# Kernel tuning notes

Hardware: AMD Instinct MI355X
Metric: run time of the kernel (lower is better)

The kernel has to match this reference:

```python
import jax, jax.numpy as jnp
import numpy as np

B, L, C, H, W = 4, 4096, 1024, 16, 512
D = C // H            # head_dim = 64
STRIDE = W // 2


def setup_inputs() -> dict:
    key = jax.random.key(0)
    k0, k1, k2 = jax.random.split(key, 3)
    s = 0.02
    return {
        "x": jax.random.normal(k0, (B, L, C), jnp.float32),
        "w_qkv": jax.random.normal(k1, (C, 3 * C), jnp.float32) * s,
        "b_qkv": jnp.zeros((3 * C,), jnp.float32),
        "w_out": jax.random.normal(k2, (C, C), jnp.float32) * s,
        "b_out": jnp.zeros((C,), jnp.float32),
    }


def _local_attention(x, w_qkv, b_qkv, w_out, b_out):
    b, l, c = x.shape
    pad = (-l) % W  # pad seq to multiple of window_size (0 here)
    x = jnp.pad(x, ((0, 0), (0, pad), (0, 0)))
    lp = l + pad
    qkv = (x @ w_qkv + b_qkv).reshape(b, lp, 3, H, D).transpose(2, 0, 3, 1, 4)
    q, k, v = qkv[0], qkv[1], qkv[2]  # each [B, H, Lp, D]
    nw = (lp - W) // STRIDE + 1       # number of overlapping windows
    # window token indices [nw, W]
    idx = jnp.arange(nw)[:, None] * STRIDE + jnp.arange(W)[None, :]
    qw = q[:, :, idx, :]  # [B, H, nw, W, D]
    kw = k[:, :, idx, :]
    vw = v[:, :, idx, :]
    # non-causal (bidirectional=True) attention within each window,
    # flash-attn default softmax scale = head_dim**-0.5
    scores = jnp.einsum('bhnqd,bhnkd->bhnqk', qw, kw) / jnp.sqrt(jnp.float32(D))
    probs = jax.nn.softmax(scores, axis=-1)
    ow = jnp.einsum('bhnqk,bhnkd->bhnqd', probs, vw)  # [B, H, nw, W, D]
    # concatenate window outputs along sequence, back to [B, nw*W, C]
    o = ow.transpose(0, 2, 3, 1, 4).reshape(b, nw * W, c)
    o = o @ w_out + b_out
    return o[:, :l, :]


def reference(x, w_qkv, b_qkv, w_out, b_out):
    return _local_attention(x, w_qkv, b_qkv, w_out, b_out)
```

## Files before the change

### kernel.cpp

```cpp
#include <hip/hip_runtime.h>

#define LQ 2304

typedef __attribute__((ext_vector_type(8))) short bf16x8;
typedef __attribute__((ext_vector_type(8))) unsigned short u16x8;
typedef __attribute__((ext_vector_type(4))) float f32x4;
typedef __attribute__((ext_vector_type(4))) unsigned int u32x4;

#define MFMA(a, b, c) __builtin_amdgcn_mfma_f32_16x16x32_bf16((a), (b), (c), 0, 0, 0)
#define AS1 __attribute__((address_space(1)))
#define AS3 __attribute__((address_space(3)))

static __device__ __forceinline__ unsigned short f2bf(float f) {
  unsigned int u = __builtin_bit_cast(unsigned int, f);
  u += 0x7fffu + ((u >> 16) & 1u);
  return (unsigned short)(u >> 16);
}

static __device__ __forceinline__ unsigned int pkbf(float hi, float lo) {
  return __builtin_amdgcn_perm(__builtin_bit_cast(unsigned int, hi),
                               __builtin_bit_cast(unsigned int, lo), 0x07060302u);
}

static __device__ __forceinline__ void lds16(const unsigned short* g, unsigned short* l) {
  __builtin_amdgcn_global_load_lds((AS1 const unsigned int*)g, (AS3 unsigned int*)l, 16, 0, 0);
}

static __device__ __forceinline__ void transpose_body(const float* __restrict__ src,
                                                      unsigned short* __restrict__ dst,
                                                      int K, int N, int bx, int by, int tid,
                                                      float (*t)[33]) {
  int bn = bx * 32, bk = by * 32;
  int tx = tid & 31, ty = tid >> 5;
  for (int i = ty; i < 32; i += 8)
    t[i][tx] = src[(size_t)(bk + i) * N + bn + tx];
  __syncthreads();
  for (int i = ty; i < 32; i += 8)
    dst[(size_t)(bn + i) * K + bk + tx] = f2bf(t[tx][i]);
}

__global__ __launch_bounds__(256) void preprocess(const float* __restrict__ x,
                                                  unsigned short* __restrict__ xbf,
                                                  const float* __restrict__ wqkv,
                                                  unsigned short* __restrict__ wqkvT,
                                                  const float* __restrict__ wout,
                                                  unsigned short* __restrict__ woutT) {
  __shared__ float t[32][33];
  int bid = blockIdx.x, tid = threadIdx.x;
  if (bid < 4608) {
    int idx = bid * 256 + tid;
    int b = idx / 294912;
    int g = idx - b * 294912;
    int row = g >> 7, c8 = (g & 127) * 8;
    const float* src = x + ((size_t)b * 4096 + row) * 1024 + c8;
    float4 f0 = *(const float4*)src;
    float4 f1 = *(const float4*)(src + 4);
    u16x8 u;
    u[0] = f2bf(f0.x); u[1] = f2bf(f0.y); u[2] = f2bf(f0.z); u[3] = f2bf(f0.w);
    u[4] = f2bf(f1.x); u[5] = f2bf(f1.y); u[6] = f2bf(f1.z); u[7] = f2bf(f1.w);
    *(u16x8*)(xbf + ((size_t)b * 2304 + row) * 1024 + c8) = u;
  } else if (bid < 7680) {
    int tb = bid - 4608;
    transpose_body(wqkv, wqkvT, 1024, 3072, tb % 96, tb / 96, tid, t);
  } else {
    int tb = bid - 7680;
    transpose_body(wout, woutT, 1024, 1024, tb & 31, tb >> 5, tid, t);
  }
}

#define K2SCALE 0.18033688011112042f
__global__ __launch_bounds__(256) void qkv_gemm(const unsigned short* __restrict__ xbf,
                                                const float* __restrict__ bqkv,
                                                const unsigned short* __restrict__ wT,
                                                unsigned short* __restrict__ qws,
                                                unsigned short* __restrict__ kws,
                                                unsigned short* __restrict__ vws) {
  __shared__ __align__(16) unsigned short As[128 * 64];
  __shared__ __align__(16) unsigned short Bs[128 * 64];
  const int tid = threadIdx.x;
  const int mt = blockIdx.y;
  const int nt = blockIdx.x;
  const int bidx = mt / 18;
  const int l0 = (mt % 18) * 128;
  const int n0 = nt * 128;
  const int lane = tid & 63, wv = tid >> 6;
  const int wm = (wv >> 1) * 64, wn = (wv & 1) * 64;
  const int l16 = lane & 15, quad = lane >> 4;

  const int srow = lane >> 3;
  const int sc = ((lane & 7) ^ srow) * 8;
  const unsigned short* ga = xbf + ((size_t)(bidx * LQ + l0 + wv * 32 + srow)) * 1024 + sc;
  const unsigned short* gb = wT + ((size_t)(n0 + wv * 32 + srow)) * 1024 + sc;
  unsigned short* la = As + wv * 2048;
  unsigned short* lb = Bs + wv * 2048;
  const int xsw = (l16 & 7) * 8;

  const f32x4 zero4 = {0.f, 0.f, 0.f, 0.f};
  f32x4 acc[4][4];
#pragma unroll
  for (int i = 0; i < 4; i++)
#pragma unroll
    for (int j = 0; j < 4; j++) acc[i][j] = zero4;

  for (int k0 = 0; k0 < 1024; k0 += 64) {
    __syncthreads();
#pragma unroll
    for (int j = 0; j < 4; j++) {
      lds16(ga + j * 8 * 1024, la + j * 512);
      lds16(gb + j * 8 * 1024, lb + j * 512);
    }
    __syncthreads();
#pragma unroll
    for (int h = 0; h < 2; h++) {
      bf16x8 af[4], bfv[4];
#pragma unroll
      for (int i = 0; i < 4; i++)
        af[i] = *(const bf16x8*)(&As[(wm + i * 16 + l16) * 64 + (((h << 5) + quad * 8) ^ xsw)]);
#pragma unroll
      for (int j = 0; j < 4; j++)
        bfv[j] = *(const bf16x8*)(&Bs[(wn + j * 16 + l16) * 64 + (((h << 5) + quad * 8) ^ xsw)]);
#pragma unroll
      for (int i = 0; i < 4; i++)
#pragma unroll
        for (int j = 0; j < 4; j++)
          acc[i][j] = MFMA(af[i], bfv[j], acc[i][j]);
    }
    ga += 64;
    gb += 64;
  }

#pragma unroll
  for (int j = 0; j < 4; j++) {
    int col = n0 + wn + j * 16 + l16;
    int which = col >> 10;
    int hcol = (col >> 6) & 15;
    int dcol = col & 63;
    unsigned short* dst = which == 0 ? qws : (which == 1 ? kws : vws);
    float scale = which == 0 ? K2SCALE : 1.0f;
    float bias = bqkv[col];
    size_t cbase = ((size_t)bidx * 16 + hcol) * LQ * 64 + dcol;
#pragma unroll
    for (int i = 0; i < 4; i++) {
      int lrow = l0 + wm + i * 16 + quad * 4;
#pragma unroll
      for (int r = 0; r < 4; r++)
        dst[cbase + (size_t)(lrow + r) * 64] = f2bf((acc[i][j][r] + bias) * scale);
    }
  }
}

#define KSTR 72
#define VSTRT 136

__global__ __launch_bounds__(512, 2) void attn_kernel(const unsigned short* __restrict__ q,
                                                      const unsigned short* __restrict__ k,
                                                      const unsigned short* __restrict__ v,
                                                      unsigned short* __restrict__ o) {
  __shared__ __align__(16) unsigned short Ks[128 * KSTR];
  __shared__ __align__(16) unsigned short Vt[64 * VSTRT];
  const int n = blockIdx.x, h = blockIdx.y, b = blockIdx.z;
  const size_t base = (((size_t)b * 16 + h) * LQ + n * 256) * 64;
  const unsigned short* qg = q + base;
  const unsigned short* kg = k + base;
  const unsigned short* vg = v + base;
  const int tid = threadIdx.x;
  const int lane = tid & 63, wv = tid >> 6;
  const int l16 = lane & 15, quad = lane >> 4;
  const f32x4 zero4 = {0.f, 0.f, 0.f, 0.f};
  const float RB = 0.002815015607053277f;

  bf16x8 qf0[4], qf1[4];
#pragma unroll
  for (int qs = 0; qs < 4; qs++) {
    int qrow = wv * 64 + qs * 16 + l16;
    qf0[qs] = *(const bf16x8*)(qg + (size_t)qrow * 64 + quad * 8);
    qf1[qs] = *(const bf16x8*)(qg + (size_t)qrow * 64 + quad * 8 + 32);
  }
  f32x4 O[4][4];
#pragma unroll
  for (int qs = 0; qs < 4; qs++)
#pragma unroll
    for (int dt = 0; dt < 4; dt++) O[qs][dt] = zero4;
  float lsum[4] = {0.f, 0.f, 0.f, 0.f};

  for (int kt = 0; kt < 4; kt++) {
    __syncthreads();
#pragma unroll
    for (int it = 0; it < 2; it++) {
      int i = it * 512 + tid;
      int key = i >> 3, part = i & 7;
      *(u16x8*)(&Ks[key * KSTR + part * 8]) =
          *(const u16x8*)(kg + (size_t)(kt * 128 + key) * 64 + part * 8);
    }
#pragma unroll
    for (int it = 0; it < 2; it++) {
      int key = it * 64 + lane;
      u16x8 raw = *(const u16x8*)(vg + (size_t)(kt * 128 + key) * 64 + wv * 8);
      int pos = (key & ~31) + ((key >> 2) & 3) * 8 + ((key >> 4) & 1) * 4 + (key & 3);
#pragma unroll
      for (int t = 0; t < 8; t++) Vt[(wv * 8 + t) * VSTRT + pos] = raw[t];
    }
    __syncthreads();

    for (int c = 0; c < 4; c++) {
      const unsigned short* kr0 = &Ks[(c * 32 + l16) * KSTR + quad * 8];
      bf16x8 ka0 = *(const bf16x8*)kr0;
      bf16x8 ka1 = *(const bf16x8*)(kr0 + 32);
      bf16x8 kb0 = *(const bf16x8*)(kr0 + 16 * KSTR);
      bf16x8 kb1 = *(const bf16x8*)(kr0 + 16 * KSTR + 32);
      bf16x8 vf[4];
#pragma unroll
      for (int dt = 0; dt < 4; dt++)
        vf[dt] = *(const bf16x8*)(&Vt[(dt * 16 + l16) * VSTRT + c * 32 + quad * 8]);
#pragma unroll
      for (int qs = 0; qs < 4; qs++) {
        f32x4 s0 = zero4, s1 = zero4;
        s0 = MFMA(ka0, qf0[qs], s0);
        s0 = MFMA(ka1, qf1[qs], s0);
        s1 = MFMA(kb0, qf0[qs], s1);
        s1 = MFMA(kb1, qf1[qs], s1);
        float p0[4], p1[4], ls = 0.f;
#pragma unroll
        for (int r = 0; r < 4; r++) {
          p0[r] = __builtin_amdgcn_exp2f(s0[r] + RB);
          p1[r] = __builtin_amdgcn_exp2f(s1[r] + RB);
          ls += p0[r] + p1[r];
        }
        lsum[qs] += ls;
        u32x4 pw;
        pw[0] = pkbf(p0[1], p0[0]);
        pw[1] = pkbf(p0[3], p0[2]);
        pw[2] = pkbf(p1[1], p1[0]);
        pw[3] = pkbf(p1[3], p1[2]);
        bf16x8 pf = __builtin_bit_cast(bf16x8, pw);
#pragma unroll
        for (int dt = 0; dt < 4; dt++)
          O[qs][dt] = MFMA(pf, vf[dt], O[qs][dt]);
      }
    }
  }

#pragma unroll
  for (int qs = 0; qs < 4; qs++) {
    float ls = lsum[qs];
    ls += __shfl_xor(ls, 16);
    ls += __shfl_xor(ls, 32);
    float linv = 1.0f / ls;
    float li[4];
#pragma unroll
    for (int r = 0; r < 4; r++) li[r] = __shfl(linv, quad * 4 + r);
    size_t orow = (size_t)b * 4096 + n * 512 + wv * 64 + qs * 16;
#pragma unroll
    for (int dt = 0; dt < 4; dt++) {
      int col = h * 64 + dt * 16 + l16;
#pragma unroll
      for (int r = 0; r < 4; r++)
        o[(orow + quad * 4 + r) * 1024 + col] = f2bf(O[qs][dt][r] * li[r]);
    }
  }
}

__global__ __launch_bounds__(256) void out_gemm(const unsigned short* __restrict__ A,
                                                const unsigned short* __restrict__ wT,
                                                const float* __restrict__ bout,
                                                float* __restrict__ out) {
  __shared__ __align__(16) unsigned short As[128 * 64];
  __shared__ __align__(16) unsigned short Bs[128 * 64];
  const int tid = threadIdx.x;
  const int m0 = blockIdx.y * 128;
  const int n0 = blockIdx.x * 128;
  const int lane = tid & 63, wv = tid >> 6;
  const int wm = (wv >> 1) * 64, wn = (wv & 1) * 64;
  const int l16 = lane & 15, quad = lane >> 4;

  const int srow = lane >> 3;
  const int sc = ((lane & 7) ^ srow) * 8;
  const unsigned short* ga = A + ((size_t)(m0 + wv * 32 + srow)) * 1024 + sc;
  const unsigned short* gb = wT + ((size_t)(n0 + wv * 32 + srow)) * 1024 + sc;
  unsigned short* la = As + wv * 2048;
  unsigned short* lb = Bs + wv * 2048;
  const int xsw = (l16 & 7) * 8;

  const f32x4 zero4 = {0.f, 0.f, 0.f, 0.f};
  f32x4 acc[4][4];
#pragma unroll
  for (int i = 0; i < 4; i++)
#pragma unroll
    for (int j = 0; j < 4; j++) acc[i][j] = zero4;

  for (int k0 = 0; k0 < 1024; k0 += 64) {
    __syncthreads();
#pragma unroll
    for (int j = 0; j < 4; j++) {
      lds16(ga + j * 8 * 1024, la + j * 512);
      lds16(gb + j * 8 * 1024, lb + j * 512);
    }
    __syncthreads();
#pragma unroll
    for (int h = 0; h < 2; h++) {
      bf16x8 af[4], bfv[4];
#pragma unroll
      for (int i = 0; i < 4; i++)
        af[i] = *(const bf16x8*)(&As[(wm + i * 16 + l16) * 64 + (((h << 5) + quad * 8) ^ xsw)]);
#pragma unroll
      for (int j = 0; j < 4; j++)
        bfv[j] = *(const bf16x8*)(&Bs[(wn + j * 16 + l16) * 64 + (((h << 5) + quad * 8) ^ xsw)]);
#pragma unroll
      for (int i = 0; i < 4; i++)
#pragma unroll
        for (int j = 0; j < 4; j++)
          acc[i][j] = MFMA(af[i], bfv[j], acc[i][j]);
    }
    ga += 64;
    gb += 64;
  }

#pragma unroll
  for (int j = 0; j < 4; j++) {
    int col = n0 + wn + j * 16 + l16;
    float bias = bout[col];
#pragma unroll
    for (int i = 0; i < 4; i++) {
      int row = m0 + wm + i * 16 + quad * 4;
#pragma unroll
      for (int r = 0; r < 4; r++)
        out[(size_t)(row + r) * 1024 + col] = acc[i][j][r] + bias;
    }
  }
}

#define WQKVT_OFF 0u
#define WOUTT_OFF (WQKVT_OFF + 3072u * 1024u * 2u)
#define QWS_OFF   (WOUTT_OFF + 1024u * 1024u * 2u)
#define KVQ_SZ    (4u * 16u * 2304u * 64u * 2u)
#define KWS_OFF   (QWS_OFF + KVQ_SZ)
#define VWS_OFF   (KWS_OFF + KVQ_SZ)
#define OWS_OFF   (VWS_OFF + KVQ_SZ)
#define XBF_OFF   OWS_OFF

extern "C" void kernel_launch(void* const* d_in, const int* in_sizes, int n_in,
                              void* d_out, int out_size, void* d_ws, size_t ws_size,
                              hipStream_t stream) {
  const float* x     = (const float*)d_in[0];
  const float* w_qkv = (const float*)d_in[1];
  const float* b_qkv = (const float*)d_in[2];
  const float* w_out = (const float*)d_in[3];
  const float* b_out = (const float*)d_in[4];
  float* out = (float*)d_out;
  char* ws = (char*)d_ws;

  unsigned short* wqkvT = (unsigned short*)(ws + WQKVT_OFF);
  unsigned short* woutT = (unsigned short*)(ws + WOUTT_OFF);
  unsigned short* qws   = (unsigned short*)(ws + QWS_OFF);
  unsigned short* kws   = (unsigned short*)(ws + KWS_OFF);
  unsigned short* vws   = (unsigned short*)(ws + VWS_OFF);
  unsigned short* ows   = (unsigned short*)(ws + OWS_OFF);
  unsigned short* xbf   = (unsigned short*)(ws + XBF_OFF);

  preprocess<<<8704, 256, 0, stream>>>(x, xbf, w_qkv, wqkvT, w_out, woutT);

  qkv_gemm<<<dim3(24, 72), 256, 0, stream>>>(xbf, b_qkv, wqkvT, qws, kws, vws);

  attn_kernel<<<dim3(8, 16, 4), 512, 0, stream>>>(qws, kws, vws, ows);

  out_gemm<<<dim3(8, 128), 256, 0, stream>>>(ows, woutT, b_out, out);
}
```

Before: 325.7 us.

## Pre-swizzle K/V/O layouts in global memory and double-buffer attention with async LDS loads

The QKV GEMM epilogue now writes K with an XOR-swizzled row layout and V pre-transposed and swizzled, so the attention kernel can copy K and V tiles straight into LDS with direct global-to-LDS loads. The old per-element transpose scatter into LDS goes away. Attention moves to 1024-thread blocks that each cover a full 512-key window, using 256-key tiles, double buffering and 128KB of dynamic LDS. It writes O in a head-major swizzled layout, so the output GEMM's A tile becomes one contiguous copy. In exchange, the three kernels are tightly coupled through the layout, 128KB of LDS per block likely limits occupancy to one block per CU, and the V epilogue makes scattered 8-byte stores.

New measurement: 465.4 us. 1.43x slower.

```diff
diff --git a/kernel.cpp b/kernel.cpp
--- a/kernel.cpp
+++ b/kernel.cpp
@@ -111,14 +111,14 @@
     }
     __syncthreads();
 #pragma unroll
-    for (int h = 0; h < 2; h++) {
+    for (int kh = 0; kh < 2; kh++) {
       bf16x8 af[4], bfv[4];
 #pragma unroll
       for (int i = 0; i < 4; i++)
-        af[i] = *(const bf16x8*)(&As[(wm + i * 16 + l16) * 64 + (((h << 5) + quad * 8) ^ xsw)]);
+        af[i] = *(const bf16x8*)(&As[(wm + i * 16 + l16) * 64 + (((kh << 5) + quad * 8) ^ xsw)]);
 #pragma unroll
       for (int j = 0; j < 4; j++)
-        bfv[j] = *(const bf16x8*)(&Bs[(wn + j * 16 + l16) * 64 + (((h << 5) + quad * 8) ^ xsw)]);
+        bfv[j] = *(const bf16x8*)(&Bs[(wn + j * 16 + l16) * 64 + (((kh << 5) + quad * 8) ^ xsw)]);
 #pragma unroll
       for (int i = 0; i < 4; i++)
 #pragma unroll
@@ -135,85 +135,115 @@
     int which = col >> 10;
     int hcol = (col >> 6) & 15;
     int dcol = col & 63;
-    unsigned short* dst = which == 0 ? qws : (which == 1 ? kws : vws);
-    float scale = which == 0 ? K2SCALE : 1.0f;
     float bias = bqkv[col];
-    size_t cbase = ((size_t)bidx * 16 + hcol) * LQ * 64 + dcol;
-#pragma unroll
-    for (int i = 0; i < 4; i++) {
-      int lrow = l0 + wm + i * 16 + quad * 4;
-#pragma unroll
-      for (int r = 0; r < 4; r++)
-        dst[cbase + (size_t)(lrow + r) * 64] = f2bf((acc[i][j][r] + bias) * scale);
-    }
-  }
-}
-
-#define KSTR 72
-#define VSTRT 136
-
-__global__ __launch_bounds__(512, 2) void attn_kernel(const unsigned short* __restrict__ q,
-                                                      const unsigned short* __restrict__ k,
-                                                      const unsigned short* __restrict__ v,
-                                                      unsigned short* __restrict__ o) {
-  __shared__ __align__(16) unsigned short Ks[128 * KSTR];
-  __shared__ __align__(16) unsigned short Vt[64 * VSTRT];
-  const int n = blockIdx.x, h = blockIdx.y, b = blockIdx.z;
-  const size_t base = (((size_t)b * 16 + h) * LQ + n * 256) * 64;
-  const unsigned short* qg = q + base;
-  const unsigned short* kg = k + base;
-  const unsigned short* vg = v + base;
+    size_t bh = (size_t)bidx * 16 + hcol;
+    if (which == 0) {
+      size_t cbase = bh * 2304 * 64 + dcol;
+#pragma unroll
+      for (int i = 0; i < 4; i++) {
+        int key0 = l0 + wm + i * 16 + quad * 4;
+#pragma unroll
+        for (int r = 0; r < 4; r++)
+          qws[cbase + (size_t)(key0 + r) * 64] = f2bf((acc[i][j][r] + bias) * K2SCALE);
+      }
+    } else if (which == 1) {
+#pragma unroll
+      for (int i = 0; i < 4; i++) {
+        int key0 = l0 + wm + i * 16 + quad * 4;
+#pragma unroll
+        for (int r = 0; r < 4; r++) {
+          int key = key0 + r;
+          size_t addr = (bh * 2304 + key) * 64 + (((dcol >> 3) ^ (key & 7)) << 3) + (dcol & 7);
+          kws[addr] = f2bf(acc[i][j][r] + bias);
+        }
+      }
+    } else {
+      size_t rowb = (bh * 64 + dcol) * 2304;
+#pragma unroll
+      for (int i = 0; i < 4; i++) {
+        int key0 = l0 + wm + i * 16 + quad * 4;
+        int pos = ((key0 >> 5) & 3) * 32 + ((key0 >> 2) & 3) * 8 + ((key0 >> 4) & 1) * 4;
+        int kk = (key0 & ~127) + (((pos >> 3) ^ (dcol & 7)) << 3) + (pos & 7);
+        ushort4 u;
+        u.x = f2bf(acc[i][j][0] + bias);
+        u.y = f2bf(acc[i][j][1] + bias);
+        u.z = f2bf(acc[i][j][2] + bias);
+        u.w = f2bf(acc[i][j][3] + bias);
+        *(ushort4*)(vws + rowb + kk) = u;
+      }
+    }
+  }
+}
+
+#define ATTN_LDS 131072
+
+__global__ __launch_bounds__(1024, 4) void attn_kernel(const unsigned short* __restrict__ q,
+                                                       const unsigned short* __restrict__ k,
+                                                       const unsigned short* __restrict__ v,
+                                                       unsigned short* __restrict__ o) {
+  extern __shared__ unsigned short lds[];
+  const int bid = blockIdx.x;
+  const int n = bid >> 6, bh = bid & 63;
+  const int b = bh >> 4, h = bh & 15;
+  const unsigned short* qg = q + ((size_t)bh * 2304 + n * 256) * 64;
+  const unsigned short* kg = k + ((size_t)bh * 2304 + n * 256) * 64;
+  const unsigned short* vgb = v + (size_t)bh * 64 * 2304 + n * 256;
   const int tid = threadIdx.x;
   const int lane = tid & 63, wv = tid >> 6;
   const int l16 = lane & 15, quad = lane >> 4;
+  const int xs = l16 & 7;
   const f32x4 zero4 = {0.f, 0.f, 0.f, 0.f};
   const float RB = 0.002815015607053277f;
 
-  bf16x8 qf0[4], qf1[4];
-#pragma unroll
-  for (int qs = 0; qs < 4; qs++) {
-    int qrow = wv * 64 + qs * 16 + l16;
+  auto stage = [&](int kt, int buf) {
+    const unsigned short* kgt = kg + kt * 256 * 64;
+    unsigned short* kb = lds + buf * 16384;
+    lds16(kgt + (wv * 64 + lane) * 8, kb + wv * 512);
+    lds16(kgt + (1024 + wv * 64 + lane) * 8, kb + 8192 + wv * 512);
+    unsigned short* vb = lds + 32768 + buf * 16384;
+    const unsigned short* vgt = vgb + kt * 256;
+    int d0 = wv * 2;
+    lds16(vgt + (size_t)(d0 + (lane >> 5)) * 2304 + (lane & 31) * 8, vb + d0 * 256);
+    int d1 = 32 + wv * 2;
+    lds16(vgt + (size_t)(d1 + (lane >> 5)) * 2304 + (lane & 31) * 8, vb + d1 * 256);
+  };
+
+  bf16x8 qf0[2], qf1[2];
+#pragma unroll
+  for (int qs = 0; qs < 2; qs++) {
+    int qrow = wv * 32 + qs * 16 + l16;
     qf0[qs] = *(const bf16x8*)(qg + (size_t)qrow * 64 + quad * 8);
     qf1[qs] = *(const bf16x8*)(qg + (size_t)qrow * 64 + quad * 8 + 32);
   }
-  f32x4 O[4][4];
-#pragma unroll
-  for (int qs = 0; qs < 4; qs++)
+  f32x4 O[2][4];
+#pragma unroll
+  for (int qs = 0; qs < 2; qs++)
 #pragma unroll
     for (int dt = 0; dt < 4; dt++) O[qs][dt] = zero4;
-  float lsum[4] = {0.f, 0.f, 0.f, 0.f};
-
-  for (int kt = 0; kt < 4; kt++) {
-    __syncthreads();
-#pragma unroll
-    for (int it = 0; it < 2; it++) {
-      int i = it * 512 + tid;
-      int key = i >> 3, part = i & 7;
-      *(u16x8*)(&Ks[key * KSTR + part * 8]) =
-          *(const u16x8*)(kg + (size_t)(kt * 128 + key) * 64 + part * 8);
-    }
-#pragma unroll
-    for (int it = 0; it < 2; it++) {
-      int key = it * 64 + lane;
-      u16x8 raw = *(const u16x8*)(vg + (size_t)(kt * 128 + key) * 64 + wv * 8);
-      int pos = (key & ~31) + ((key >> 2) & 3) * 8 + ((key >> 4) & 1) * 4 + (key & 3);
-#pragma unroll
-      for (int t = 0; t < 8; t++) Vt[(wv * 8 + t) * VSTRT + pos] = raw[t];
-    }
-    __syncthreads();
-
-    for (int c = 0; c < 4; c++) {
-      const unsigned short* kr0 = &Ks[(c * 32 + l16) * KSTR + quad * 8];
-      bf16x8 ka0 = *(const bf16x8*)kr0;
-      bf16x8 ka1 = *(const bf16x8*)(kr0 + 32);
-      bf16x8 kb0 = *(const bf16x8*)(kr0 + 16 * KSTR);
-      bf16x8 kb1 = *(const bf16x8*)(kr0 + 16 * KSTR + 32);
+  float lsum[2] = {0.f, 0.f};
+
+  stage(0, 0);
+  for (int kt = 0; kt < 2; kt++) {
+    __syncthreads();
+    if (kt == 0) stage(1, 1);
+    const unsigned short* KB = lds + kt * 16384;
+    const unsigned short* VB = lds + 32768 + kt * 16384;
+    const int ca = (quad ^ xs) << 3, cb = ((4 + quad) ^ xs) << 3;
+#pragma unroll
+    for (int c = 0; c < 8; c++) {
+      const unsigned short* krow0 = KB + (c * 32 + l16) * 64;
+      const unsigned short* krow1 = krow0 + 16 * 64;
+      bf16x8 ka0 = *(const bf16x8*)(krow0 + ca);
+      bf16x8 ka1 = *(const bf16x8*)(krow0 + cb);
+      bf16x8 kb0 = *(const bf16x8*)(krow1 + ca);
+      bf16x8 kb1 = *(const bf16x8*)(krow1 + cb);
+      int vco = (c >> 2) * 128 + ((((c & 3) * 4 + quad) ^ xs) << 3);
       bf16x8 vf[4];
 #pragma unroll
       for (int dt = 0; dt < 4; dt++)
-        vf[dt] = *(const bf16x8*)(&Vt[(dt * 16 + l16) * VSTRT + c * 32 + quad * 8]);
-#pragma unroll
-      for (int qs = 0; qs < 4; qs++) {
+        vf[dt] = *(const bf16x8*)(VB + (dt * 16 + l16) * 256 + vco);
+#pragma unroll
+      for (int qs = 0; qs < 2; qs++) {
         f32x4 s0 = zero4, s1 = zero4;
         s0 = MFMA(ka0, qf0[qs], s0);
         s0 = MFMA(ka1, qf1[qs], s0);
@@ -235,27 +265,28 @@
         bf16x8 pf = __builtin_bit_cast(bf16x8, pw);
 #pragma unroll
         for (int dt = 0; dt < 4; dt++)
-          O[qs][dt] = MFMA(pf, vf[dt], O[qs][dt]);
+          O[qs][dt] = MFMA(vf[dt], pf, O[qs][dt]);
       }
     }
   }
 
 #pragma unroll
-  for (int qs = 0; qs < 4; qs++) {
+  for (int qs = 0; qs < 2; qs++) {
     float ls = lsum[qs];
     ls += __shfl_xor(ls, 16);
     ls += __shfl_xor(ls, 32);
     float linv = 1.0f / ls;
-    float li[4];
-#pragma unroll
-    for (int r = 0; r < 4; r++) li[r] = __shfl(linv, quad * 4 + r);
-    size_t orow = (size_t)b * 4096 + n * 512 + wv * 64 + qs * 16;
+    size_t gr = (size_t)b * 4096 + n * 512 + wv * 32 + qs * 16 + l16;
+    unsigned short* ob = o + ((size_t)h * 16384 + gr) * 64 + (quad & 1) * 4;
 #pragma unroll
     for (int dt = 0; dt < 4; dt++) {
-      int col = h * 64 + dt * 16 + l16;
-#pragma unroll
-      for (int r = 0; r < 4; r++)
-        o[(orow + quad * 4 + r) * 1024 + col] = f2bf(O[qs][dt][r] * li[r]);
+      int ch = (((2 * dt + (quad >> 1)) ^ xs) << 3);
+      ushort4 u;
+      u.x = f2bf(O[qs][dt][0] * linv);
+      u.y = f2bf(O[qs][dt][1] * linv);
+      u.z = f2bf(O[qs][dt][2] * linv);
+      u.w = f2bf(O[qs][dt][3] * linv);
+      *(ushort4*)(ob + ch) = u;
     }
   }
 }
@@ -273,11 +304,10 @@
   const int wm = (wv >> 1) * 64, wn = (wv & 1) * 64;
   const int l16 = lane & 15, quad = lane >> 4;
 
+  const unsigned short* ga = A + (size_t)m0 * 64;
   const int srow = lane >> 3;
   const int sc = ((lane & 7) ^ srow) * 8;
-  const unsigned short* ga = A + ((size_t)(m0 + wv * 32 + srow)) * 1024 + sc;
   const unsigned short* gb = wT + ((size_t)(n0 + wv * 32 + srow)) * 1024 + sc;
-  unsigned short* la = As + wv * 2048;
   unsigned short* lb = Bs + wv * 2048;
   const int xsw = (l16 & 7) * 8;
 
@@ -288,30 +318,30 @@
 #pragma unroll
     for (int j = 0; j < 4; j++) acc[i][j] = zero4;
 
-  for (int k0 = 0; k0 < 1024; k0 += 64) {
+  for (int kk = 0; kk < 16; kk++) {
     __syncthreads();
 #pragma unroll
     for (int j = 0; j < 4; j++) {
-      lds16(ga + j * 8 * 1024, la + j * 512);
+      lds16(ga + (j * 256 + wv * 64 + lane) * 8, As + (j * 256 + wv * 64) * 8);
       lds16(gb + j * 8 * 1024, lb + j * 512);
     }
     __syncthreads();
 #pragma unroll
-    for (int h = 0; h < 2; h++) {
+    for (int kh = 0; kh < 2; kh++) {
       bf16x8 af[4], bfv[4];
 #pragma unroll
       for (int i = 0; i < 4; i++)
-        af[i] = *(const bf16x8*)(&As[(wm + i * 16 + l16) * 64 + (((h << 5) + quad * 8) ^ xsw)]);
+        af[i] = *(const bf16x8*)(&As[(wm + i * 16 + l16) * 64 + (((kh << 5) + quad * 8) ^ xsw)]);
 #pragma unroll
       for (int j = 0; j < 4; j++)
-        bfv[j] = *(const bf16x8*)(&Bs[(wn + j * 16 + l16) * 64 + (((h << 5) + quad * 8) ^ xsw)]);
+        bfv[j] = *(const bf16x8*)(&Bs[(wn + j * 16 + l16) * 64 + (((kh << 5) + quad * 8) ^ xsw)]);
 #pragma unroll
       for (int i = 0; i < 4; i++)
 #pragma unroll
         for (int j = 0; j < 4; j++)
           acc[i][j] = MFMA(af[i], bfv[j], acc[i][j]);
     }
-    ga += 64;
+    ga += 16384 * 64;
     gb += 64;
   }
 
@@ -361,7 +391,9 @@
 
   qkv_gemm<<<dim3(24, 72), 256, 0, stream>>>(xbf, b_qkv, wqkvT, qws, kws, vws);
 
-  attn_kernel<<<dim3(8, 16, 4), 512, 0, stream>>>(qws, kws, vws, ows);
+  (void)hipFuncSetAttribute((const void*)attn_kernel,
+                            hipFuncAttributeMaxDynamicSharedMemorySize, ATTN_LDS);
+  attn_kernel<<<512, 1024, ATTN_LDS, stream>>>(qws, kws, vws, ows);
 
   out_gemm<<<dim3(8, 128), 256, 0, stream>>>(ows, woutT, b_out, out);
 }
```
